# Optimization experiments

Hardware: AMD Instinct MI355X
Metric: run time of the kernel (lower is better)

The kernel has to match this reference:

```python
import jax, jax.numpy as jnp
import numpy as np

N_NODES = 50000
N_EDGES = 800000
N_RELS = 32
D_IN = 64
D_OUT = 64


def setup_inputs() -> dict:
    key = jax.random.key(0)
    k_feat, k_w, k_src, k_dst, k_et = jax.random.split(key, 5)
    feat = jax.random.normal(k_feat, (N_NODES, D_IN), dtype=jnp.float32)
    weight = jax.random.normal(k_w, (N_RELS, D_IN, D_OUT), dtype=jnp.float32) * 0.05
    src = jax.random.randint(k_src, (N_EDGES,), 0, N_NODES, dtype=jnp.int32)
    dst = jax.random.randint(k_dst, (N_EDGES,), 0, N_NODES, dtype=jnp.int32)
    etypes = jax.random.randint(k_et, (N_EDGES,), 0, N_RELS, dtype=jnp.int32)
    # per-relation edge counts (unused by the unsorted math, kept for API fidelity)
    E_per_rel = jnp.bincount(etypes, length=N_RELS)
    return {"feat": feat, "weight": weight, "src": src, "dst": dst,
            "etypes": etypes, "E_per_rel": E_per_rel}


def reference(feat, weight, src, dst, etypes, E_per_rel):
    # out[d] = sum_{e: dst[e]==d} feat[src[e]] @ weight[etypes[e]]
    # Since the per-edge matmul is linear in feat, we first segment-sum the
    # gathered source features by (dst, etype), then apply each relation's
    # weight once. This avoids materializing an [E, D_IN, D_OUT] tensor.
    N = feat.shape[0]
    R, D_in, D_out = weight.shape
    gathered = feat[src]                                   # [E, D_in]
    seg = dst.astype(jnp.int32) * R + etypes.astype(jnp.int32)  # [E]
    per_node_rel = jax.ops.segment_sum(gathered, seg, num_segments=N * R)
    per_node_rel = per_node_rel.reshape(N, R, D_in)        # [N, R, D_in]
    out = jnp.einsum('nri,rio->no', per_node_rel, weight)  # [N, D_out]
    return out
```

## Files before the change

kernel.cpp:

```cpp
#include <hip/hip_runtime.h>
#include <hip/hip_bf16.h>

#define N_NODES 50000
#define N_EDGES 800000
#define N_RELS  32
#define D       64
#define TILE_M  256
#define NBKT    196
#define EPB     2048
#define NEBLK   ((N_EDGES + EPB - 1) / EPB)

typedef _Float16 half8 __attribute__((ext_vector_type(8)));
typedef float    f32x4 __attribute__((ext_vector_type(4)));

#define OFF_RELHIST 0u
#define OFF_BKTHIST 128u
#define OFF_RELCUR  1024u
#define OFF_BKTCUR  1152u
#define OFF_ROFF    1936u
#define OFF_TB      2080u
#define OFF_BKTOFF  2224u
#define OFF_DSTOFF  3072u
#define OFF_RELSRC  203776u
#define OFF_CSRY    3403776u
#define OFF_WT      6603776u
#define OFF_FEATH   6865920u
#define OFF_Y_FULL  13265920u
#define OFF_Y_BASE  6865920u
#define WS_FULL     115665920u
#define WS_BASE     109265920u

__global__ __launch_bounds__(256) void rgcn_edge_atomic(
    const float* __restrict__ feat, const float* __restrict__ weight,
    const int* __restrict__ src, const int* __restrict__ dst,
    const int* __restrict__ et, float* __restrict__ out, int nquads)
{
    const int tid  = blockIdx.x * blockDim.x + threadIdx.x;
    const int wave = tid >> 6, lane = tid & 63;
    const int grp = lane >> 4, lg = lane & 15;
    const int wave_stride = (gridDim.x * blockDim.x) >> 6;
    for (int q = wave; q < nquads; q += wave_stride) {
        const int e = q * 4 + grp;
        const int s = src[e], d = dst[e], r = et[e];
        const float* w = weight + (size_t)r * D * D + lg * 4;
        float ax = 0.f, ay = 0.f, az = 0.f, aw = 0.f;
        #pragma unroll
        for (int i4 = 0; i4 < D / 4; ++i4) {
            const float4 f  = *reinterpret_cast<const float4*>(feat + (size_t)s * D + i4 * 4);
            const float4 w0 = *reinterpret_cast<const float4*>(w + (i4 * 4 + 0) * D);
            const float4 w1 = *reinterpret_cast<const float4*>(w + (i4 * 4 + 1) * D);
            const float4 w2 = *reinterpret_cast<const float4*>(w + (i4 * 4 + 2) * D);
            const float4 w3 = *reinterpret_cast<const float4*>(w + (i4 * 4 + 3) * D);
            ax += f.x*w0.x; ay += f.x*w0.y; az += f.x*w0.z; aw += f.x*w0.w;
            ax += f.y*w1.x; ay += f.y*w1.y; az += f.y*w1.z; aw += f.y*w1.w;
            ax += f.z*w2.x; ay += f.z*w2.y; az += f.z*w2.z; aw += f.z*w2.w;
            ax += f.w*w3.x; ay += f.w*w3.y; az += f.w*w3.z; aw += f.w*w3.w;
        }
        float* orow = out + (size_t)d * D + lg * 4;
        atomicAdd(orow + 0, ax); atomicAdd(orow + 1, ay);
        atomicAdd(orow + 2, az); atomicAdd(orow + 3, aw);
    }
}

__global__ __launch_bounds__(256) void k0_wt(const float* __restrict__ w,
                                             _Float16* __restrict__ wT)
{
    const int r = blockIdx.x, t = threadIdx.x;
    #pragma unroll
    for (int i = 0; i < 16; ++i) {
        int oidx = i * 256 + t;
        int o = oidx >> 6, k = oidx & 63;
        wT[(size_t)r * 4096 + oidx] = (_Float16)w[(size_t)r * 4096 + k * 64 + o];
    }
}

__global__ __launch_bounds__(256) void kF_feath(const float* __restrict__ feat,
                                                _Float16* __restrict__ featH)
{
    const int base = (blockIdx.x * 256 + threadIdx.x) * 8;
    if (base >= N_NODES * D) return;
    float4 f0 = *reinterpret_cast<const float4*>(feat + base);
    float4 f1 = *reinterpret_cast<const float4*>(feat + base + 4);
    half8 h;
    h[0]=(_Float16)f0.x; h[1]=(_Float16)f0.y; h[2]=(_Float16)f0.z; h[3]=(_Float16)f0.w;
    h[4]=(_Float16)f1.x; h[5]=(_Float16)f1.y; h[6]=(_Float16)f1.z; h[7]=(_Float16)f1.w;
    *reinterpret_cast<half8*>(featH + base) = h;
}

__global__ __launch_bounds__(256) void kA_hist(const int* __restrict__ et,
                                               const int* __restrict__ dst,
                                               int* __restrict__ relhist,
                                               int* __restrict__ bkthist)
{
    __shared__ int lh[N_RELS];
    __shared__ int lb[NBKT];
    const int t = threadIdx.x;
    if (t < N_RELS) lh[t] = 0;
    if (t < NBKT)   lb[t] = 0;
    __syncthreads();
    const int base = blockIdx.x * EPB + t * 8;
    #pragma unroll
    for (int i = 0; i < 8; ++i) {
        int e = base + i;
        if (e < N_EDGES) {
            atomicAdd(&lh[et[e]], 1);
            atomicAdd(&lb[dst[e] >> 8], 1);
        }
    }
    __syncthreads();
    if (t < N_RELS && lh[t]) atomicAdd(&relhist[t], lh[t]);
    if (t < NBKT   && lb[t]) atomicAdd(&bkthist[t], lb[t]);
}

__global__ __launch_bounds__(256) void kB_scan(const int* __restrict__ relhist,
                                               const int* __restrict__ bkthist,
                                               int* __restrict__ roff,
                                               int* __restrict__ relcur,
                                               int* __restrict__ tb,
                                               int* __restrict__ bktoff,
                                               int* __restrict__ bktcur,
                                               int* __restrict__ dst_off)
{
    __shared__ int s[256];
    const int t = threadIdx.x;
    int v = (t < N_RELS) ? relhist[t] : 0;
    s[t] = v; __syncthreads();
    #pragma unroll
    for (int off = 1; off < 32; off <<= 1) {
        int u = (t >= off && t < N_RELS) ? s[t - off] : 0;
        __syncthreads(); s[t] += u; __syncthreads();
    }
    if (t < N_RELS) { int ex = s[t] - v; roff[t] = ex; relcur[t] = ex; }
    if (t == N_RELS - 1) roff[N_RELS] = s[t];
    __syncthreads();
    int w = (v + TILE_M - 1) / TILE_M;
    s[t] = (t < N_RELS) ? w : 0; __syncthreads();
    #pragma unroll
    for (int off = 1; off < 32; off <<= 1) {
        int u = (t >= off && t < N_RELS) ? s[t - off] : 0;
        __syncthreads(); s[t] += u; __syncthreads();
    }
    if (t < N_RELS) tb[t] = s[t] - w;
    if (t == N_RELS - 1) tb[N_RELS] = s[t];
    __syncthreads();
    int v2 = (t < NBKT) ? bkthist[t] : 0;
    s[t] = v2; __syncthreads();
    #pragma unroll
    for (int off = 1; off < 256; off <<= 1) {
        int u = (t >= off) ? s[t - off] : 0;
        __syncthreads(); s[t] += u; __syncthreads();
    }
    if (t < NBKT) { int ex = s[t] - v2; bktoff[t] = ex; bktcur[t] = ex; }
    if (t == NBKT - 1) bktoff[NBKT] = s[t];
    if (t == 0) dst_off[N_NODES] = N_EDGES;
}

__global__ __launch_bounds__(256) void kC_scatter(const int* __restrict__ src,
                                                  const int* __restrict__ dst,
                                                  const int* __restrict__ et,
                                                  int* __restrict__ relcur,
                                                  int* __restrict__ bktcur,
                                                  int* __restrict__ relsrc,
                                                  int* __restrict__ bucketed)
{
    __shared__ int lh[N_RELS],  lbase[N_RELS];
    __shared__ int lb[NBKT],    lbase2[NBKT];
    const int t = threadIdx.x;
    if (t < N_RELS) lh[t] = 0;
    if (t < NBKT)   lb[t] = 0;
    __syncthreads();
    const int base = blockIdx.x * EPB + t * 8;
    int r_[8], b_[8], s_[8], d_[8], sl[8], sl2[8];
    #pragma unroll
    for (int i = 0; i < 8; ++i) {
        int e = base + i;
        if (e < N_EDGES) {
            r_[i] = et[e]; s_[i] = src[e]; d_[i] = dst[e];
            b_[i] = d_[i] >> 8;
            sl[i]  = atomicAdd(&lh[r_[i]], 1);
            sl2[i] = atomicAdd(&lb[b_[i]], 1);
        }
    }
    __syncthreads();
    if (t < N_RELS && lh[t]) lbase[t]  = atomicAdd(&relcur[t], lh[t]);
    if (t < NBKT   && lb[t]) lbase2[t] = atomicAdd(&bktcur[t], lb[t]);
    __syncthreads();
    #pragma unroll
    for (int i = 0; i < 8; ++i) {
        int e = base + i;
        if (e < N_EDGES) {
            int j = lbase[r_[i]] + sl[i];
            relsrc[j] = s_[i];
            bucketed[lbase2[b_[i]] + sl2[i]] = ((d_[i] & 255) << 20) | j;
        }
    }
}

__global__ __launch_bounds__(256) void kD_csr(const int* __restrict__ bucketed,
                                              const int* __restrict__ bktoff,
                                              int* __restrict__ csr_y,
                                              int* __restrict__ dst_off)
{
    __shared__ int hist[256];
    __shared__ int s[256];
    const int b = blockIdx.x, t = threadIdx.x;
    const int lo = bktoff[b], hi = bktoff[b + 1];
    hist[t] = 0; __syncthreads();
    for (int p = lo + t; p < hi; p += 256)
        atomicAdd(&hist[bucketed[p] >> 20], 1);
    __syncthreads();
    int v = hist[t];
    s[t] = v; __syncthreads();
    #pragma unroll
    for (int off = 1; off < 256; off <<= 1) {
        int u = (t >= off) ? s[t - off] : 0;
        __syncthreads(); s[t] += u; __syncthreads();
    }
    int ex = lo + s[t] - v;
    int n = b * 256 + t;
    if (n < N_NODES) dst_off[n] = ex;
    hist[t] = ex;
    __syncthreads();
    for (int p = lo + t; p < hi; p += 256) {
        int key = bucketed[p];
        int pos = atomicAdd(&hist[key >> 20], 1);
        csr_y[pos] = key & 0xFFFFF;
    }
}

template <bool USE_H>
__global__ __launch_bounds__(256) void k4_gemm(const float* __restrict__ feat,
                                               const _Float16* __restrict__ featH,
                                               const _Float16* __restrict__ wT,
                                               const int* __restrict__ relsrc,
                                               const int* __restrict__ roff,
                                               const int* __restrict__ tb,
                                               _Float16* __restrict__ Y)
{
    __shared__ _Float16 aT[TILE_M * 64];
    __shared__ _Float16 wL[64 * 64];
    const int b = blockIdx.x, t = threadIdx.x;

    int r = -1, ti = 0, t0 = 0;
    #pragma unroll
    for (int q = 0; q < N_RELS; ++q) {
        int t1 = tb[q + 1];
        if (b >= t0 && b < t1) { r = q; ti = b - t0; }
        t0 = t1;
    }
    if (r < 0) return;
    const int segstart = roff[r], segend = roff[r + 1];
    const int rowbase = segstart + ti * TILE_M;

    {
        const _Float16* wsrc = wT + (size_t)r * 4096;
        #pragma unroll
        for (int it = 0; it < 2; ++it) {
            int L8 = it * 256 + t;
            int o = L8 >> 3, kcol = (L8 & 7) * 8;
            int baddr = (o * 128 + kcol * 2) ^ ((o & 7) << 4);
            *reinterpret_cast<half8*>(reinterpret_cast<char*>(wL) + baddr) =
                *reinterpret_cast<const half8*>(wsrc + L8 * 8);
        }
    }
    {
        const int j = rowbase + t;
        const int sidx = (j < segend) ? relsrc[j] : 0;
        if (USE_H) {
            const half8* hrow = reinterpret_cast<const half8*>(featH + (size_t)sidx * 64);
            #pragma unroll
            for (int c = 0; c < 4; ++c) {
                half8 h0 = hrow[c * 2 + 0];
                half8 h1 = hrow[c * 2 + 1];
                int base = t * 128 + c * 32;
                int a0 = (base)      ^ ((t & 7) << 4);
                int a1 = (base + 16) ^ ((t & 7) << 4);
                *reinterpret_cast<half8*>(reinterpret_cast<char*>(aT) + a0) = h0;
                *reinterpret_cast<half8*>(reinterpret_cast<char*>(aT) + a1) = h1;
            }
        } else {
            const float4* frow = reinterpret_cast<const float4*>(feat + (size_t)sidx * 64);
            #pragma unroll
            for (int c = 0; c < 4; ++c) {
                float4 f0 = frow[c*4+0], f1 = frow[c*4+1], f2 = frow[c*4+2], f3 = frow[c*4+3];
                half8 h0, h1;
                h0[0]=(_Float16)f0.x; h0[1]=(_Float16)f0.y; h0[2]=(_Float16)f0.z; h0[3]=(_Float16)f0.w;
                h0[4]=(_Float16)f1.x; h0[5]=(_Float16)f1.y; h0[6]=(_Float16)f1.z; h0[7]=(_Float16)f1.w;
                h1[0]=(_Float16)f2.x; h1[1]=(_Float16)f2.y; h1[2]=(_Float16)f2.z; h1[3]=(_Float16)f2.w;
                h1[4]=(_Float16)f3.x; h1[5]=(_Float16)f3.y; h1[6]=(_Float16)f3.z; h1[7]=(_Float16)f3.w;
                int base = t * 128 + c * 32;
                int a0 = (base)      ^ ((t & 7) << 4);
                int a1 = (base + 16) ^ ((t & 7) << 4);
                *reinterpret_cast<half8*>(reinterpret_cast<char*>(aT) + a0) = h0;
                *reinterpret_cast<half8*>(reinterpret_cast<char*>(aT) + a1) = h1;
            }
        }
    }
    __syncthreads();

    const int wid = t >> 6, l = t & 63;
    const int lrow = l & 15, lkb = l >> 4;
    f32x4 acc[4][4] = {};
    #pragma unroll
    for (int ks = 0; ks < 2; ++ks) {
        half8 af[4], bfr[4];
        #pragma unroll
        for (int rt = 0; rt < 4; ++rt) {
            int row = wid * 64 + rt * 16 + lrow;
            int baddr = (row * 128 + ks * 64 + lkb * 16) ^ ((row & 7) << 4);
            af[rt] = *reinterpret_cast<const half8*>(reinterpret_cast<const char*>(aT) + baddr);
        }
        #pragma unroll
        for (int ct = 0; ct < 4; ++ct) {
            int n = ct * 16 + lrow;
            int baddr = (n * 128 + ks * 64 + lkb * 16) ^ ((n & 7) << 4);
            bfr[ct] = *reinterpret_cast<const half8*>(reinterpret_cast<const char*>(wL) + baddr);
        }
        #pragma unroll
        for (int rt = 0; rt < 4; ++rt)
            #pragma unroll
            for (int ct = 0; ct < 4; ++ct)
                acc[rt][ct] = __builtin_amdgcn_mfma_f32_16x16x32_f16(af[rt], bfr[ct], acc[rt][ct], 0, 0, 0);
    }
    #pragma unroll
    for (int rt = 0; rt < 4; ++rt) {
        int rowg = rowbase + wid * 64 + rt * 16 + (l >> 4) * 4;
        #pragma unroll
        for (int ct = 0; ct < 4; ++ct) {
            int col = ct * 16 + lrow;
            #pragma unroll
            for (int reg = 0; reg < 4; ++reg) {
                int row = rowg + reg;
                if (row < segend)
                    Y[(size_t)row * 64 + col] = (_Float16)acc[rt][ct][reg];
            }
        }
    }
}

__global__ __launch_bounds__(256) void k5_reduce(const _Float16* __restrict__ Y,
                                                 const int* __restrict__ csr_y,
                                                 const int* __restrict__ dst_off,
                                                 float* __restrict__ out)
{
    const int wid = threadIdx.x >> 6, l = threadIdx.x & 63;
    const int n = blockIdx.x * 4 + wid;
    if (n >= N_NODES) return;
    const int p0 = dst_off[n], p1 = dst_off[n + 1];
    float acc = 0.f;
    int p = p0;
    for (; p + 4 <= p1; p += 4) {
        int ja = csr_y[p], jb = csr_y[p+1], jc = csr_y[p+2], jd = csr_y[p+3];
        acc += (float)Y[(size_t)ja * 64 + l] + (float)Y[(size_t)jb * 64 + l]
             + (float)Y[(size_t)jc * 64 + l] + (float)Y[(size_t)jd * 64 + l];
    }
    for (; p < p1; ++p)
        acc += (float)Y[(size_t)csr_y[p] * 64 + l];
    out[(size_t)n * 64 + l] = acc;
}

extern "C" void kernel_launch(void* const* d_in, const int* in_sizes, int n_in,
                              void* d_out, int out_size, void* d_ws, size_t ws_size,
                              hipStream_t stream) {
    const float* feat   = (const float*)d_in[0];
    const float* weight = (const float*)d_in[1];
    const int*   src    = (const int*)d_in[2];
    const int*   dst    = (const int*)d_in[3];
    const int*   et     = (const int*)d_in[4];
    float*       out    = (float*)d_out;

    if (ws_size < (size_t)WS_BASE) {
        hipMemsetAsync(d_out, 0, (size_t)out_size * sizeof(float), stream);
        hipLaunchKernelGGL(rgcn_edge_atomic, dim3(4096), dim3(256), 0, stream,
                           feat, weight, src, dst, et, out, N_EDGES / 4);
        return;
    }
    const bool use_h = (ws_size >= (size_t)WS_FULL);

    char* ws = (char*)d_ws;
    int*       relhist  = (int*)(ws + OFF_RELHIST);
    int*       bkthist  = (int*)(ws + OFF_BKTHIST);
    int*       relcur   = (int*)(ws + OFF_RELCUR);
    int*       bktcur   = (int*)(ws + OFF_BKTCUR);
    int*       roff     = (int*)(ws + OFF_ROFF);
    int*       tb       = (int*)(ws + OFF_TB);
    int*       bktoff   = (int*)(ws + OFF_BKTOFF);
    int*       dst_off  = (int*)(ws + OFF_DSTOFF);
    int*       relsrc   = (int*)(ws + OFF_RELSRC);
    int*       csr_y    = (int*)(ws + OFF_CSRY);
    _Float16*  wT       = (_Float16*)(ws + OFF_WT);
    _Float16*  featH    = (_Float16*)(ws + OFF_FEATH);
    _Float16*  Y        = (_Float16*)(ws + (use_h ? OFF_Y_FULL : OFF_Y_BASE));
    int*       bucketed = (int*)Y;

    hipMemsetAsync(ws, 0, 912, stream);

    hipLaunchKernelGGL(k0_wt,      dim3(N_RELS), dim3(256), 0, stream, weight, wT);
    if (use_h)
        hipLaunchKernelGGL(kF_feath, dim3((N_NODES * D / 8 + 255) / 256), dim3(256), 0, stream, feat, featH);
    hipLaunchKernelGGL(kA_hist,    dim3(NEBLK),  dim3(256), 0, stream, et, dst, relhist, bkthist);
    hipLaunchKernelGGL(kB_scan,    dim3(1),      dim3(256), 0, stream, relhist, bkthist, roff, relcur, tb, bktoff, bktcur, dst_off);
    hipLaunchKernelGGL(kC_scatter, dim3(NEBLK),  dim3(256), 0, stream, src, dst, et, relcur, bktcur, relsrc, bucketed);
    hipLaunchKernelGGL(kD_csr,     dim3(NBKT),   dim3(256), 0, stream, bucketed, bktoff, csr_y, dst_off);
    const int max_tiles = N_EDGES / TILE_M + N_RELS;
    if (use_h)
        hipLaunchKernelGGL((k4_gemm<true>),  dim3(max_tiles), dim3(256), 0, stream, feat, featH, wT, relsrc, roff, tb, Y);
    else
        hipLaunchKernelGGL((k4_gemm<false>), dim3(max_tiles), dim3(256), 0, stream, feat, featH, wT, relsrc, roff, tb, Y);
    hipLaunchKernelGGL(k5_reduce,  dim3((N_NODES + 3) / 4), dim3(256), 0, stream, Y, csr_y, dst_off, out);
}
```

Measured before the change: 135.2 us.

## Scatter GEMM output rows into dst-sorted order and merge prep kernels

The GEMM kernel now writes each result row directly to its destination-sorted position via a new j2pos map, so the reduce kernel reads Y contiguously instead of gathering through csr_y indices. The tile size is halved to 128 rows, with half the threads loading features and the other half loading weights in parallel. The weight-transpose and feature-to-half kernels are merged into one launch. The trade-off is scattered row writes from the GEMM, which replace the scattered reads in the reduce, and more GEMM blocks.

```diff
diff --git a/kernel.cpp b/kernel.cpp
--- a/kernel.cpp
+++ b/kernel.cpp
@@ -5,7 +5,7 @@
 #define N_EDGES 800000
 #define N_RELS  32
 #define D       64
-#define TILE_M  256
+#define TILE_M  128
 #define NBKT    196
 #define EPB     2048
 #define NEBLK   ((N_EDGES + EPB - 1) / EPB)
@@ -22,7 +22,7 @@
 #define OFF_BKTOFF  2224u
 #define OFF_DSTOFF  3072u
 #define OFF_RELSRC  203776u
-#define OFF_CSRY    3403776u
+#define OFF_J2POS   3403776u
 #define OFF_WT      6603776u
 #define OFF_FEATH   6865920u
 #define OFF_Y_FULL  13265920u
@@ -62,29 +62,30 @@
     }
 }
 
-__global__ __launch_bounds__(256) void k0_wt(const float* __restrict__ w,
-                                             _Float16* __restrict__ wT)
-{
-    const int r = blockIdx.x, t = threadIdx.x;
-    #pragma unroll
-    for (int i = 0; i < 16; ++i) {
-        int oidx = i * 256 + t;
-        int o = oidx >> 6, k = oidx & 63;
-        wT[(size_t)r * 4096 + oidx] = (_Float16)w[(size_t)r * 4096 + k * 64 + o];
-    }
-}
-
-__global__ __launch_bounds__(256) void kF_feath(const float* __restrict__ feat,
-                                                _Float16* __restrict__ featH)
-{
-    const int base = (blockIdx.x * 256 + threadIdx.x) * 8;
-    if (base >= N_NODES * D) return;
-    float4 f0 = *reinterpret_cast<const float4*>(feat + base);
-    float4 f1 = *reinterpret_cast<const float4*>(feat + base + 4);
-    half8 h;
-    h[0]=(_Float16)f0.x; h[1]=(_Float16)f0.y; h[2]=(_Float16)f0.z; h[3]=(_Float16)f0.w;
-    h[4]=(_Float16)f1.x; h[5]=(_Float16)f1.y; h[6]=(_Float16)f1.z; h[7]=(_Float16)f1.w;
-    *reinterpret_cast<half8*>(featH + base) = h;
+__global__ __launch_bounds__(256) void kPre(const float* __restrict__ w,
+                                            _Float16* __restrict__ wT,
+                                            const float* __restrict__ feat,
+                                            _Float16* __restrict__ featH)
+{
+    const int t = threadIdx.x;
+    if (blockIdx.x < N_RELS) {
+        const int r = blockIdx.x;
+        #pragma unroll
+        for (int i = 0; i < 16; ++i) {
+            int oidx = i * 256 + t;
+            int o = oidx >> 6, k = oidx & 63;
+            wT[(size_t)r * 4096 + oidx] = (_Float16)w[(size_t)r * 4096 + k * 64 + o];
+        }
+    } else {
+        const int base = ((blockIdx.x - N_RELS) * 256 + t) * 8;
+        if (base >= N_NODES * D) return;
+        float4 f0 = *reinterpret_cast<const float4*>(feat + base);
+        float4 f1 = *reinterpret_cast<const float4*>(feat + base + 4);
+        half8 h;
+        h[0]=(_Float16)f0.x; h[1]=(_Float16)f0.y; h[2]=(_Float16)f0.z; h[3]=(_Float16)f0.w;
+        h[4]=(_Float16)f1.x; h[5]=(_Float16)f1.y; h[6]=(_Float16)f1.z; h[7]=(_Float16)f1.w;
+        *reinterpret_cast<half8*>(featH + base) = h;
+    }
 }
 
 __global__ __launch_bounds__(256) void kA_hist(const int* __restrict__ et,
@@ -198,7 +199,7 @@
 
 __global__ __launch_bounds__(256) void kD_csr(const int* __restrict__ bucketed,
                                               const int* __restrict__ bktoff,
-                                              int* __restrict__ csr_y,
+                                              int* __restrict__ j2pos,
                                               int* __restrict__ dst_off)
 {
     __shared__ int hist[256];
@@ -224,7 +225,7 @@
     for (int p = lo + t; p < hi; p += 256) {
         int key = bucketed[p];
         int pos = atomicAdd(&hist[key >> 20], 1);
-        csr_y[pos] = key & 0xFFFFF;
+        j2pos[key & 0xFFFFF] = pos;
     }
 }
 
@@ -233,12 +234,14 @@
                                                const _Float16* __restrict__ featH,
                                                const _Float16* __restrict__ wT,
                                                const int* __restrict__ relsrc,
+                                               const int* __restrict__ j2pos,
                                                const int* __restrict__ roff,
                                                const int* __restrict__ tb,
                                                _Float16* __restrict__ Y)
 {
     __shared__ _Float16 aT[TILE_M * 64];
     __shared__ _Float16 wL[64 * 64];
+    __shared__ int      ypos[TILE_M];
     const int b = blockIdx.x, t = threadIdx.x;
 
     int r = -1, ti = 0, t0 = 0;
@@ -249,23 +252,14 @@
         t0 = t1;
     }
     if (r < 0) return;
-    const int segstart = roff[r], segend = roff[r + 1];
-    const int rowbase = segstart + ti * TILE_M;
-
-    {
-        const _Float16* wsrc = wT + (size_t)r * 4096;
-        #pragma unroll
-        for (int it = 0; it < 2; ++it) {
-            int L8 = it * 256 + t;
-            int o = L8 >> 3, kcol = (L8 & 7) * 8;
-            int baddr = (o * 128 + kcol * 2) ^ ((o & 7) << 4);
-            *reinterpret_cast<half8*>(reinterpret_cast<char*>(wL) + baddr) =
-                *reinterpret_cast<const half8*>(wsrc + L8 * 8);
-        }
-    }
-    {
+    const int segend  = roff[r + 1];
+    const int rowbase = roff[r] + ti * TILE_M;
+
+    if (t < TILE_M) {
         const int j = rowbase + t;
-        const int sidx = (j < segend) ? relsrc[j] : 0;
+        const bool ok = (j < segend);
+        const int sidx = ok ? relsrc[j] : 0;
+        ypos[t] = ok ? j2pos[j] : 0;
         if (USE_H) {
             const half8* hrow = reinterpret_cast<const half8*>(featH + (size_t)sidx * 64);
             #pragma unroll
@@ -295,18 +289,29 @@
                 *reinterpret_cast<half8*>(reinterpret_cast<char*>(aT) + a1) = h1;
             }
         }
+    } else {
+        const _Float16* wsrc = wT + (size_t)r * 4096;
+        const int tt = t - 128;
+        #pragma unroll
+        for (int it = 0; it < 4; ++it) {
+            int L8 = it * 128 + tt;
+            int o = L8 >> 3, kcol = (L8 & 7) * 8;
+            int baddr = (o * 128 + kcol * 2) ^ ((o & 7) << 4);
+            *reinterpret_cast<half8*>(reinterpret_cast<char*>(wL) + baddr) =
+                *reinterpret_cast<const half8*>(wsrc + L8 * 8);
+        }
     }
     __syncthreads();
 
     const int wid = t >> 6, l = t & 63;
     const int lrow = l & 15, lkb = l >> 4;
-    f32x4 acc[4][4] = {};
+    f32x4 acc[2][4] = {};
     #pragma unroll
     for (int ks = 0; ks < 2; ++ks) {
-        half8 af[4], bfr[4];
-        #pragma unroll
-        for (int rt = 0; rt < 4; ++rt) {
-            int row = wid * 64 + rt * 16 + lrow;
+        half8 af[2], bfr[4];
+        #pragma unroll
+        for (int rt = 0; rt < 2; ++rt) {
+            int row = wid * 32 + rt * 16 + lrow;
             int baddr = (row * 128 + ks * 64 + lkb * 16) ^ ((row & 7) << 4);
             af[rt] = *reinterpret_cast<const half8*>(reinterpret_cast<const char*>(aT) + baddr);
         }
@@ -317,29 +322,28 @@
             bfr[ct] = *reinterpret_cast<const half8*>(reinterpret_cast<const char*>(wL) + baddr);
         }
         #pragma unroll
-        for (int rt = 0; rt < 4; ++rt)
+        for (int rt = 0; rt < 2; ++rt)
             #pragma unroll
             for (int ct = 0; ct < 4; ++ct)
                 acc[rt][ct] = __builtin_amdgcn_mfma_f32_16x16x32_f16(af[rt], bfr[ct], acc[rt][ct], 0, 0, 0);
     }
     #pragma unroll
-    for (int rt = 0; rt < 4; ++rt) {
-        int rowg = rowbase + wid * 64 + rt * 16 + (l >> 4) * 4;
-        #pragma unroll
-        for (int ct = 0; ct < 4; ++ct) {
-            int col = ct * 16 + lrow;
-            #pragma unroll
-            for (int reg = 0; reg < 4; ++reg) {
-                int row = rowg + reg;
-                if (row < segend)
-                    Y[(size_t)row * 64 + col] = (_Float16)acc[rt][ct][reg];
+    for (int rt = 0; rt < 2; ++rt) {
+        int lrow0 = wid * 32 + rt * 16 + (l >> 4) * 4;
+        #pragma unroll
+        for (int reg = 0; reg < 4; ++reg) {
+            int lr = lrow0 + reg;
+            if (rowbase + lr < segend) {
+                size_t yrow = (size_t)ypos[lr] * 64;
+                #pragma unroll
+                for (int ct = 0; ct < 4; ++ct)
+                    Y[yrow + ct * 16 + lrow] = (_Float16)acc[rt][ct][reg];
             }
         }
     }
 }
 
 __global__ __launch_bounds__(256) void k5_reduce(const _Float16* __restrict__ Y,
-                                                 const int* __restrict__ csr_y,
                                                  const int* __restrict__ dst_off,
                                                  float* __restrict__ out)
 {
@@ -350,12 +354,11 @@
     float acc = 0.f;
     int p = p0;
     for (; p + 4 <= p1; p += 4) {
-        int ja = csr_y[p], jb = csr_y[p+1], jc = csr_y[p+2], jd = csr_y[p+3];
-        acc += (float)Y[(size_t)ja * 64 + l] + (float)Y[(size_t)jb * 64 + l]
-             + (float)Y[(size_t)jc * 64 + l] + (float)Y[(size_t)jd * 64 + l];
+        acc += (float)Y[(size_t)(p+0) * 64 + l] + (float)Y[(size_t)(p+1) * 64 + l]
+             + (float)Y[(size_t)(p+2) * 64 + l] + (float)Y[(size_t)(p+3) * 64 + l];
     }
     for (; p < p1; ++p)
-        acc += (float)Y[(size_t)csr_y[p] * 64 + l];
+        acc += (float)Y[(size_t)p * 64 + l];
     out[(size_t)n * 64 + l] = acc;
 }
 
@@ -387,7 +390,7 @@
     int*       bktoff   = (int*)(ws + OFF_BKTOFF);
     int*       dst_off  = (int*)(ws + OFF_DSTOFF);
     int*       relsrc   = (int*)(ws + OFF_RELSRC);
-    int*       csr_y    = (int*)(ws + OFF_CSRY);
+    int*       j2pos    = (int*)(ws + OFF_J2POS);
     _Float16*  wT       = (_Float16*)(ws + OFF_WT);
     _Float16*  featH    = (_Float16*)(ws + OFF_FEATH);
     _Float16*  Y        = (_Float16*)(ws + (use_h ? OFF_Y_FULL : OFF_Y_BASE));
@@ -395,17 +398,16 @@
 
     hipMemsetAsync(ws, 0, 912, stream);
 
-    hipLaunchKernelGGL(k0_wt,      dim3(N_RELS), dim3(256), 0, stream, weight, wT);
-    if (use_h)
-        hipLaunchKernelGGL(kF_feath, dim3((N_NODES * D / 8 + 255) / 256), dim3(256), 0, stream, feat, featH);
+    const int pre_blocks = use_h ? (N_RELS + (N_NODES * D / 8 + 255) / 256) : N_RELS;
+    hipLaunchKernelGGL(kPre,       dim3(pre_blocks), dim3(256), 0, stream, weight, wT, feat, featH);
     hipLaunchKernelGGL(kA_hist,    dim3(NEBLK),  dim3(256), 0, stream, et, dst, relhist, bkthist);
     hipLaunchKernelGGL(kB_scan,    dim3(1),      dim3(256), 0, stream, relhist, bkthist, roff, relcur, tb, bktoff, bktcur, dst_off);
     hipLaunchKernelGGL(kC_scatter, dim3(NEBLK),  dim3(256), 0, stream, src, dst, et, relcur, bktcur, relsrc, bucketed);
-    hipLaunchKernelGGL(kD_csr,     dim3(NBKT),   dim3(256), 0, stream, bucketed, bktoff, csr_y, dst_off);
+    hipLaunchKernelGGL(kD_csr,     dim3(NBKT),   dim3(256), 0, stream, bucketed, bktoff, j2pos, dst_off);
     const int max_tiles = N_EDGES / TILE_M + N_RELS;
     if (use_h)
-        hipLaunchKernelGGL((k4_gemm<true>),  dim3(max_tiles), dim3(256), 0, stream, feat, featH, wT, relsrc, roff, tb, Y);
+        hipLaunchKernelGGL((k4_gemm<true>),  dim3(max_tiles), dim3(256), 0, stream, feat, featH, wT, relsrc, j2pos, roff, tb, Y);
     else
-        hipLaunchKernelGGL((k4_gemm<false>), dim3(max_tiles), dim3(256), 0, stream, feat, featH, wT, relsrc, roff, tb, Y);
-    hipLaunchKernelGGL(k5_reduce,  dim3((N_NODES + 3) / 4), dim3(256), 0, stream, Y, csr_y, dst_off, out);
-}
+        hipLaunchKernelGGL((k4_gemm<false>), dim3(max_tiles), dim3(256), 0, stream, feat, featH, wT, relsrc, j2pos, roff, tb, Y);
+    hipLaunchKernelGGL(k5_reduce,  dim3((N_NODES + 3) / 4), dim3(256), 0, stream, Y, dst_off, out);
+}
```

New measurement: 119.5 us. -11.7%, faster.
